# Kernel tuning notes

Measured on AMD Instinct MI355X. Metric: run time of the kernel, lower is better.

## Reference

```python
import jax, jax.numpy as jnp
import numpy as np

B = 8           # hardcoded batchsize in the original forward
EPS = 1e-4      # scn.BatchNormalization default eps


def setup_inputs() -> dict:
    key = jax.random.key(0)
    ks = jax.random.split(key, 8)
    Nq, Nkv = 16384, 32768
    dec_in, enc_in, nf = 64, 64, 128
    nbr = jax.random.randint(ks[2], (Nq, 27), 0, Nq, dtype=jnp.int32)
    # center tap of the 3x3x3 submanifold conv is the point itself
    nbr = nbr.at[:, 13].set(jnp.arange(Nq, dtype=jnp.int32))
    return {
        "x_decoder_feat": jax.random.normal(ks[0], (Nq, dec_in), jnp.float32),
        "x_encoder_feat": jax.random.normal(ks[1], (Nkv, enc_in), jnp.float32),
        "nbr_idx": nbr,
        "W_p1": jax.random.normal(ks[3], (27, dec_in, nf), jnp.float32) * 0.05,
        "W_q": jax.random.normal(ks[4], (nf, nf), jnp.float32) * 0.05,
        "W_k": jax.random.normal(ks[5], (enc_in, nf), jnp.float32) * 0.05,
        "W_v": jax.random.normal(ks[6], (enc_in, nf), jnp.float32) * 0.05,
        "W_trans": jax.random.normal(ks[7], (nf, nf), jnp.float32) * 0.05,
        "gamma": jnp.ones((nf,), jnp.float32),
        "beta": jnp.zeros((nf,), jnp.float32),
    }


def reference(x_decoder_feat, x_encoder_feat, nbr_idx, W_p1, W_q, W_k, W_v,
              W_trans, gamma, beta):
    nf = W_q.shape[1]
    # p1: 3x3x3 submanifold conv = gather 27 neighbors, per-offset matmul, sum
    x_dec = jnp.einsum('nkc,kcf->nf', x_decoder_feat[nbr_idx], W_p1)  # [Nq,nf]
    q = (x_dec @ W_q).reshape(B, -1, nf)            # [B, nq, nf]
    k = (x_encoder_feat @ W_k).reshape(B, -1, nf)   # [B, nkv, nf]
    v = (x_encoder_feat @ W_v).reshape(B, -1, nf)
    # per-batch QK^T softmax V (no 1/sqrt(d) scaling in original)
    attn = jax.nn.softmax(jnp.einsum('bqc,bkc->bqk', q, k), axis=-1)
    x_r = jnp.einsum('bqk,bkc->bqc', attn, v).reshape(-1, nf)  # [Nq,nf]
    # trans_conv (1x1) + batchnorm (batch stats over all points)
    t = x_r @ W_trans
    mean = t.mean(axis=0)
    var = t.var(axis=0)
    bn = (t - mean) * jax.lax.rsqrt(var + EPS) * gamma + beta
    return x_dec + bn
```

## Files before the change

### kernel.cpp

```cpp
#include <hip/hip_runtime.h>
#include <math.h>

#define NQ      16384
#define NKV     32768
#define CIN     64
#define NF      128
#define NOFF    27
#define BATCH   8
#define SQ      2048
#define SKV     4096
#define BN_EPS  1e-4f
#define SPLIT   4
#define KV_PER_SPLIT (SKV / SPLIT)
#define TILES_PER_SPLIT (KV_PER_SPLIT / 64)
#define LOG2E   1.4426950408889634f
#define SHIFT2  57.70780163555854f

typedef unsigned short u16;
typedef unsigned int   u32;
typedef __attribute__((ext_vector_type(4))) float f32x4;
typedef __attribute__((ext_vector_type(8))) short s16x8;

__device__ __forceinline__ u16 f2b(float x) {
    union { float f; unsigned u; } c; c.f = x;
    unsigned r = (c.u + 0x7FFFu + ((c.u >> 16) & 1u)) >> 16;
    return (u16)r;
}
__device__ __forceinline__ float b2f(u16 x) {
    union { unsigned u; float f; } c; c.u = ((unsigned)x) << 16;
    return c.f;
}
__device__ __forceinline__ u32 pk2bf(float lo, float hi) {
    union { float f; u32 u; } a, b;
    a.f = lo; b.f = hi;
    return __builtin_amdgcn_perm(b.u + 0x8000u, a.u + 0x8000u, 0x07060302u);
}
__device__ __forceinline__ void g2l16(const void* gp, void* lp) {
    __builtin_amdgcn_global_load_lds(
        (const __attribute__((address_space(1))) unsigned*)gp,
        (__attribute__((address_space(3))) unsigned*)lp, 16, 0, 0);
}

__device__ __forceinline__ void wtrans_one(
    const float* __restrict__ src, u16* __restrict__ dst, int K, int id, float sc)
{
    int n  = id / (K / 4);
    int k4 = (id % (K / 4)) * 4;
    const float* s = src + (size_t)k4 * NF + n;
    ushort4 o;
    o.x = f2b(s[0] * sc); o.y = f2b(s[NF] * sc);
    o.z = f2b(s[2 * NF] * sc); o.w = f2b(s[3 * NF] * sc);
    *(ushort4*)(dst + (size_t)n * K + k4) = o;
}

__global__ __launch_bounds__(256) void prep_kernel(
    const float* __restrict__ xdec_feat, const float* __restrict__ Wp1,
    const float* __restrict__ Wq, const float* __restrict__ Wk,
    const float* __restrict__ Wv, const float* __restrict__ Wt,
    u16* __restrict__ xf_bf, u16* __restrict__ wp1t,
    u16* __restrict__ wqT, u16* __restrict__ wkT,
    u16* __restrict__ wvT, u16* __restrict__ wtT,
    float* __restrict__ stats)
{
    int bid = blockIdx.x;
    int t   = threadIdx.x;
    if (bid < 1024) {
        int i = (bid * 256 + t) * 4;
        float4 v = *(const float4*)(xdec_feat + i);
        ushort4 o;
        o.x = f2b(v.x); o.y = f2b(v.y); o.z = f2b(v.z); o.w = f2b(v.w);
        *(ushort4*)(xf_bf + i) = o;
    } else if (bid < 1240) {
        int id = (bid - 1024) * 256 + t;
        int ko = id >> 11;
        int r  = id & 2047;
        int f  = r >> 4;
        int c4 = (r & 15) * 4;
        const float* s = Wp1 + (size_t)ko * 8192 + (size_t)c4 * NF + f;
        ushort4 o;
        o.x = f2b(s[0]); o.y = f2b(s[NF]); o.z = f2b(s[2 * NF]); o.w = f2b(s[3 * NF]);
        *(ushort4*)(wp1t + (size_t)ko * 8192 + (size_t)f * 64 + c4) = o;
    } else if (bid < 1288) {
        int id = (bid - 1240) * 256 + t;
        if (id < 4096)        wtrans_one(Wq, wqT, 128, id, LOG2E);
        else if (id < 6144)   wtrans_one(Wk, wkT, 64, id - 4096, 1.f);
        else if (id < 8192)   wtrans_one(Wv, wvT, 64, id - 6144, 1.f);
        else                  wtrans_one(Wt, wtT, 128, id - 8192, 1.f);
    } else {
        stats[t] = 0.f;
    }
}

__global__ __launch_bounds__(256) void main_fused_kernel(
    const float* __restrict__ xenc, const u16* __restrict__ xf,
    const int* __restrict__ nbr, const u16* __restrict__ wp1t,
    const u16* __restrict__ wqT, const u16* __restrict__ wkT,
    const u16* __restrict__ wvT,
    u16* __restrict__ kbuf, u16* __restrict__ vt,
    float* __restrict__ xdec, u16* __restrict__ qbuf)
{
    __shared__ u16 Bs[2][128][64];
    __shared__ int nbr_s[64][28];

    const int t    = threadIdx.x;
    const int w    = t >> 6;
    const int lane = t & 63;
    const int quad = lane >> 4;
    const int l15  = lane & 15;

    if (blockIdx.x < 512) {
        const int m0 = blockIdx.x * 64 + w * 16;
        const float* Ap = xenc + (size_t)(m0 + l15) * CIN + quad * 8;
        float4 a0 = *(const float4*)(Ap);
        float4 a1 = *(const float4*)(Ap + 4);
        float4 a2 = *(const float4*)(Ap + 32);
        float4 a3 = *(const float4*)(Ap + 36);
        union { u16 a[8]; s16x8 v; } p0, p1;
        p0.a[0] = f2b(a0.x); p0.a[1] = f2b(a0.y); p0.a[2] = f2b(a0.z); p0.a[3] = f2b(a0.w);
        p0.a[4] = f2b(a1.x); p0.a[5] = f2b(a1.y); p0.a[6] = f2b(a1.z); p0.a[7] = f2b(a1.w);
        p1.a[0] = f2b(a2.x); p1.a[1] = f2b(a2.y); p1.a[2] = f2b(a2.z); p1.a[3] = f2b(a2.w);
        p1.a[4] = f2b(a3.x); p1.a[5] = f2b(a3.y); p1.a[6] = f2b(a3.z); p1.a[7] = f2b(a3.w);
        s16x8 af0 = p0.v, af1 = p1.v;

        int m  = m0 + quad * 4;
        int bb = m >> 12;
        int kv = m & 4095;
        #pragma unroll
        for (int nt = 0; nt < 8; nt++) {
            f32x4 ka = (f32x4)0.f, va = (f32x4)0.f;
            const u16* Kp = wkT + (size_t)(nt * 16 + l15) * CIN + quad * 8;
            const u16* Vp = wvT + (size_t)(nt * 16 + l15) * CIN + quad * 8;
            s16x8 kb0 = *(const s16x8*)(Kp);
            s16x8 kb1 = *(const s16x8*)(Kp + 32);
            s16x8 vb0 = *(const s16x8*)(Vp);
            s16x8 vb1 = *(const s16x8*)(Vp + 32);
            ka = __builtin_amdgcn_mfma_f32_16x16x32_bf16(af0, kb0, ka, 0, 0, 0);
            ka = __builtin_amdgcn_mfma_f32_16x16x32_bf16(af1, kb1, ka, 0, 0, 0);
            va = __builtin_amdgcn_mfma_f32_16x16x32_bf16(af0, vb0, va, 0, 0, 0);
            va = __builtin_amdgcn_mfma_f32_16x16x32_bf16(af1, vb1, va, 0, 0, 0);
            #pragma unroll
            for (int r = 0; r < 4; r++)
                kbuf[(size_t)(m0 + quad * 4 + r) * NF + nt * 16 + l15] = f2b(ka[r]);
            ushort4 pk;
            pk.x = f2b(va[0]); pk.y = f2b(va[1]); pk.z = f2b(va[2]); pk.w = f2b(va[3]);
            *(ushort4*)(vt + (size_t)(bb * NF + nt * 16 + l15) * SKV + kv) = pk;
        }
        return;
    }

    const int base = (blockIdx.x - 512) * 64;

    for (int i = t; i < 64 * NOFF; i += 256)
        nbr_s[i / NOFF][i % NOFF] = nbr[(size_t)base * NOFF + i];

    f32x4 oacc[8];
    #pragma unroll
    for (int n = 0; n < 8; n++) oacc[n] = (f32x4)0.f;

    const int arow = w * 16 + l15;
    const int sr   = w * 32 + (lane >> 3);

    #pragma unroll
    for (int c = 0; c < 4; c++) {
        int row = sr + c * 8;
        int kk  = (lane & 7) ^ (row & 7);
        g2l16(wp1t + (size_t)row * 64 + kk * 8, &Bs[0][w * 32 + c * 8][0]);
    }
    __syncthreads();

    for (int ko = 0; ko < NOFF; ko++) {
        int cur = ko & 1;
        if (ko + 1 < NOFF) {
            int nxt = (ko + 1) & 1;
            #pragma unroll
            for (int c = 0; c < 4; c++) {
                int row = sr + c * 8;
                int kk  = (lane & 7) ^ (row & 7);
                g2l16(wp1t + (size_t)(ko + 1) * 8192 + (size_t)row * 64 + kk * 8,
                      &Bs[nxt][w * 32 + c * 8][0]);
            }
        }
        int nb = nbr_s[arow][ko];
        const u16* ap = xf + (size_t)nb * CIN + quad * 8;
        s16x8 af0 = *(const s16x8*)(ap);
        s16x8 af1 = *(const s16x8*)(ap + 32);
        #pragma unroll
        for (int nt = 0; nt < 8; nt++) {
            int pc0 = quad ^ (l15 & 7);
            int pc1 = (4 + quad) ^ (l15 & 7);
            s16x8 bf0 = *(const s16x8*)&Bs[cur][nt * 16 + l15][pc0 * 8];
            s16x8 bf1 = *(const s16x8*)&Bs[cur][nt * 16 + l15][pc1 * 8];
            oacc[nt] = __builtin_amdgcn_mfma_f32_16x16x32_bf16(af0, bf0, oacc[nt], 0, 0, 0);
            oacc[nt] = __builtin_amdgcn_mfma_f32_16x16x32_bf16(af1, bf1, oacc[nt], 0, 0, 0);
        }
        __syncthreads();
    }

    u16* xq = &Bs[0][0][0];
    #pragma unroll
    for (int nt = 0; nt < 8; nt++)
        #pragma unroll
        for (int r = 0; r < 4; r++) {
            int row = w * 16 + quad * 4 + r;
            int col = nt * 16 + l15;
            xdec[(size_t)(base + row) * NF + col] = oacc[nt][r];
            xq[row * 136 + col] = f2b(oacc[nt][r]);
        }

    s16x8 aq[4];
    #pragma unroll
    for (int ks = 0; ks < 4; ks++)
        aq[ks] = *(const s16x8*)&xq[(w * 16 + l15) * 136 + ks * 32 + quad * 8];

    #pragma unroll
    for (int nt = 0; nt < 8; nt++) {
        f32x4 acc = (f32x4)0.f;
        const u16* Wp = wqT + (size_t)(nt * 16 + l15) * NF + quad * 8;
        #pragma unroll
        for (int ks = 0; ks < 4; ks++) {
            s16x8 bf = *(const s16x8*)(Wp + ks * 32);
            acc = __builtin_amdgcn_mfma_f32_16x16x32_bf16(aq[ks], bf, acc, 0, 0, 0);
        }
        #pragma unroll
        for (int r = 0; r < 4; r++)
            qbuf[(size_t)(base + w * 16 + quad * 4 + r) * NF + nt * 16 + l15] = f2b(acc[r]);
    }
}

__global__ __launch_bounds__(256) void attn_mfma_kernel(
    const u16* __restrict__ Q, const u16* __restrict__ K,
    const u16* __restrict__ Vt, u16* __restrict__ Opart,
    float* __restrict__ lpart)
{
    __shared__ u16 Ks[2][64][128];
    __shared__ u16 Vs[2][128][64];
    __shared__ u16 Ps[4][16][72];

    const int t    = threadIdx.x;
    const int b    = blockIdx.y;
    const int q0   = blockIdx.x * 128;
    const int sp   = blockIdx.z;
    const int w    = t >> 6;
    const int lane = t & 63;
    const int quad = lane >> 4;
    const int l15  = lane & 15;

    const u16* Kb  = K  + (size_t)b * SKV * NF;
    const u16* Vtb = Vt + (size_t)b * NF * SKV;

    s16x8 qf[2][4];
    #pragma unroll
    for (int g = 0; g < 2; g++) {
        const u16* Qp = Q + ((size_t)(b * SQ + q0 + w * 32 + g * 16 + l15)) * NF + quad * 8;
        #pragma unroll
        for (int ks = 0; ks < 4; ks++) qf[g][ks] = *(const s16x8*)(Qp + ks * 32);
    }

    f32x4 oacc[2][8];
    #pragma unroll
    for (int g = 0; g < 2; g++)
        #pragma unroll
        for (int n = 0; n < 8; n++) oacc[g][n] = (f32x4)0.f;
    float lrow[2] = {0.f, 0.f};

    const int kvbase = sp * KV_PER_SPLIT;
    const int krow = w * 16 + (lane >> 4);
    const int vrow = w * 32 + (lane >> 3);

    #pragma unroll
    for (int c = 0; c < 4; c++) {
        int row = krow + c * 4;
        int k8  = (lane & 15) ^ (row & 15);
        g2l16(Kb + (size_t)(kvbase + row) * NF + k8 * 8, &Ks[0][w * 16 + c * 4][0]);
    }
    #pragma unroll
    for (int c = 0; c < 4; c++) {
        int row = vrow + c * 8;
        int k8  = (lane & 7) ^ (row & 7);
        g2l16(Vtb + (size_t)row * SKV + kvbase + k8 * 8, &Vs[0][w * 32 + c * 8][0]);
    }

    for (int tile = 0; tile < TILES_PER_SPLIT; tile++) {
        const int cur = tile & 1;
        __syncthreads();
        if (tile + 1 < TILES_PER_SPLIT) {
            const int nxt = (tile + 1) & 1;
            int kvn = kvbase + (tile + 1) * 64;
            #pragma unroll
            for (int c = 0; c < 4; c++) {
                int row = krow + c * 4;
                int k8  = (lane & 15) ^ (row & 15);
                g2l16(Kb + (size_t)(kvn + row) * NF + k8 * 8, &Ks[nxt][w * 16 + c * 4][0]);
            }
            #pragma unroll
            for (int c = 0; c < 4; c++) {
                int row = vrow + c * 8;
                int k8  = (lane & 7) ^ (row & 7);
                g2l16(Vtb + (size_t)row * SKV + kvn + k8 * 8, &Vs[nxt][w * 32 + c * 8][0]);
            }
        }

        f32x4 sacc[2][4];
        #pragma unroll
        for (int c = 0; c < 4; c++) {
            sacc[0][c] = (f32x4)0.f;
            sacc[1][c] = (f32x4)0.f;
            #pragma unroll
            for (int ks = 0; ks < 4; ks++) {
                int p = (ks * 4 + quad) ^ l15;
                s16x8 ka = *(const s16x8*)&Ks[cur][c * 16 + l15][p * 8];
                sacc[0][c] = __builtin_amdgcn_mfma_f32_16x16x32_bf16(ka, qf[0][ks], sacc[0][c], 0, 0, 0);
                sacc[1][c] = __builtin_amdgcn_mfma_f32_16x16x32_bf16(ka, qf[1][ks], sacc[1][c], 0, 0, 0);
            }
        }

        s16x8 pb[2][2];
        #pragma unroll
        for (int g = 0; g < 2; g++) {
            float rs = 0.f;
            float pv[4][4];
            #pragma unroll
            for (int c = 0; c < 4; c++)
                #pragma unroll
                for (int r = 0; r < 4; r++) {
                    float p = exp2f(sacc[g][c][r] - SHIFT2);
                    pv[c][r] = p;
                    rs += p;
                }
            rs += __shfl_xor(rs, 16);
            rs += __shfl_xor(rs, 32);
            lrow[g] += rs;
            #pragma unroll
            for (int c = 0; c < 4; c++) {
                uint2 pk;
                pk.x = pk2bf(pv[c][0], pv[c][1]);
                pk.y = pk2bf(pv[c][2], pv[c][3]);
                *(uint2*)&Ps[w][l15][c * 16 + quad * 4] = pk;
            }
            pb[g][0] = *(const s16x8*)&Ps[w][l15][quad * 8];
            pb[g][1] = *(const s16x8*)&Ps[w][l15][32 + quad * 8];
        }

        #pragma unroll
        for (int mt = 0; mt < 8; mt++) {
            int p0 = quad ^ (l15 & 7);
            int p1 = (4 + quad) ^ (l15 & 7);
            s16x8 va0 = *(const s16x8*)&Vs[cur][mt * 16 + l15][p0 * 8];
            s16x8 va1 = *(const s16x8*)&Vs[cur][mt * 16 + l15][p1 * 8];
            oacc[0][mt] = __builtin_amdgcn_mfma_f32_16x16x32_bf16(va0, pb[0][0], oacc[0][mt], 0, 0, 0);
            oacc[0][mt] = __builtin_amdgcn_mfma_f32_16x16x32_bf16(va1, pb[0][1], oacc[0][mt], 0, 0, 0);
            oacc[1][mt] = __builtin_amdgcn_mfma_f32_16x16x32_bf16(va0, pb[1][0], oacc[1][mt], 0, 0, 0);
            oacc[1][mt] = __builtin_amdgcn_mfma_f32_16x16x32_bf16(va1, pb[1][1], oacc[1][mt], 0, 0, 0);
        }
    }

    #pragma unroll
    for (int g = 0; g < 2; g++) {
        int grow = b * SQ + q0 + w * 32 + g * 16 + l15;
        u16* Ob = Opart + (size_t)sp * NQ * NF + (size_t)grow * NF;
        #pragma unroll
        for (int mt = 0; mt < 8; mt++) {
            uint2 ov;
            ov.x = pk2bf(oacc[g][mt][0], oacc[g][mt][1]);
            ov.y = pk2bf(oacc[g][mt][2], oacc[g][mt][3]);
            *(uint2*)(Ob + mt * 16 + quad * 4) = ov;
        }
        if (quad == 0) lpart[sp * NQ + grow] = lrow[g];
    }
}

__global__ __launch_bounds__(256) void tgemm_fused_kernel(
    const u16* __restrict__ Opart, const float* __restrict__ lpart,
    const u16* __restrict__ WT, float* __restrict__ C, float* __restrict__ stats)
{
    const int t    = threadIdx.x;
    const int w    = t >> 6;
    const int lane = t & 63;
    const int quad = lane >> 4;
    const int l15  = lane & 15;
    const int m0   = blockIdx.x * 64 + w * 16;
    const int row  = m0 + l15;

    float L = 0.f;
    #pragma unroll
    for (int s = 0; s < SPLIT; s++) L += lpart[s * NQ + row];
    float invL = 1.f / L;

    s16x8 af[4];
    #pragma unroll
    for (int ks = 0; ks < 4; ks++) {
        float sum[8] = {0.f, 0.f, 0.f, 0.f, 0.f, 0.f, 0.f, 0.f};
        #pragma unroll
        for (int s = 0; s < SPLIT; s++) {
            const u16* p = Opart + (size_t)s * NQ * NF + (size_t)row * NF + ks * 32 + quad * 8;
            ushort4 u0 = *(const ushort4*)p;
            ushort4 u1 = *(const ushort4*)(p + 4);
            sum[0] += b2f(u0.x); sum[1] += b2f(u0.y);
            sum[2] += b2f(u0.z); sum[3] += b2f(u0.w);
            sum[4] += b2f(u1.x); sum[5] += b2f(u1.y);
            sum[6] += b2f(u1.z); sum[7] += b2f(u1.w);
        }
        union { u16 a[8]; s16x8 v; } pk;
        #pragma unroll
        for (int j = 0; j < 8; j++) pk.a[j] = f2b(sum[j] * invL);
        af[ks] = pk.v;
    }

    f32x4 oacc[8];
    #pragma unroll
    for (int nt = 0; nt < 8; nt++) {
        oacc[nt] = (f32x4)0.f;
        const u16* Wp = WT + (size_t)(nt * 16 + l15) * NF + quad * 8;
        #pragma unroll
        for (int ks = 0; ks < 4; ks++) {
            s16x8 bf = *(const s16x8*)(Wp + ks * 32);
            oacc[nt] = __builtin_amdgcn_mfma_f32_16x16x32_bf16(af[ks], bf, oacc[nt], 0, 0, 0);
        }
    }

    float s[8], sq[8];
    #pragma unroll
    for (int nt = 0; nt < 8; nt++) {
        s[nt] = 0.f; sq[nt] = 0.f;
        #pragma unroll
        for (int r = 0; r < 4; r++) {
            float v = oacc[nt][r];
            C[(size_t)(m0 + quad * 4 + r) * NF + nt * 16 + l15] = v;
            s[nt] += v; sq[nt] += v * v;
        }
    }
    #pragma unroll
    for (int nt = 0; nt < 8; nt++) {
        s[nt]  += __shfl_xor(s[nt], 16);  s[nt]  += __shfl_xor(s[nt], 32);
        sq[nt] += __shfl_xor(sq[nt], 16); sq[nt] += __shfl_xor(sq[nt], 32);
    }
    __shared__ float red[2][4][128];
    if (quad == 0) {
        #pragma unroll
        for (int nt = 0; nt < 8; nt++) {
            red[0][w][nt * 16 + l15] = s[nt];
            red[1][w][nt * 16 + l15] = sq[nt];
        }
    }
    __syncthreads();
    if (t < 128) {
        float a = red[0][0][t] + red[0][1][t] + red[0][2][t] + red[0][3][t];
        atomicAdd(&stats[t], a);
    } else if (t < 256) {
        int f = t - 128;
        float a = red[1][0][f] + red[1][1][f] + red[1][2][f] + red[1][3][f];
        atomicAdd(&stats[128 + f], a);
    }
}

__global__ __launch_bounds__(256) void bn_finalize(
    const float* __restrict__ tbuf, const float* __restrict__ xdec,
    const float* __restrict__ stats, const float* __restrict__ gamma,
    const float* __restrict__ beta, float* __restrict__ out)
{
    const int g = blockIdx.x * 256 + threadIdx.x;
    const int e = g * 4;
    const int f = e & (NF - 1);
    const float invN = 1.0f / (float)NQ;
    float4 tv = *(const float4*)(tbuf + e);
    float4 xv = *(const float4*)(xdec + e);
    float o[4], tt[4] = {tv.x, tv.y, tv.z, tv.w}, xx[4] = {xv.x, xv.y, xv.z, xv.w};
    #pragma unroll
    for (int u = 0; u < 4; u++) {
        float sum  = stats[f + u];
        float sumq = stats[128 + f + u];
        float mean = sum * invN;
        float var  = sumq * invN - mean * mean;
        float sc   = rsqrtf(var + BN_EPS) * gamma[f + u];
        o[u] = xx[u] + (tt[u] - mean) * sc + beta[f + u];
    }
    float4 ov = make_float4(o[0], o[1], o[2], o[3]);
    *(float4*)(out + e) = ov;
}

extern "C" void kernel_launch(void* const* d_in, const int* in_sizes, int n_in,
                              void* d_out, int out_size, void* d_ws, size_t ws_size,
                              hipStream_t stream) {
    const float* xdec_feat = (const float*)d_in[0];
    const float* xenc_feat = (const float*)d_in[1];
    const int*   nbr       = (const int*)d_in[2];
    const float* Wp1       = (const float*)d_in[3];
    const float* Wq        = (const float*)d_in[4];
    const float* Wk        = (const float*)d_in[5];
    const float* Wv        = (const float*)d_in[6];
    const float* Wt        = (const float*)d_in[7];
    const float* gamma     = (const float*)d_in[8];
    const float* beta      = (const float*)d_in[9];
    float* out = (float*)d_out;

    char* wsb = (char*)d_ws;
    const size_t MB = 1024 * 1024;
    float* xdec   = (float*)(wsb + 0);
    u16*   qbuf   = (u16*)  (wsb + 8 * MB);
    u16*   kbuf   = (u16*)  (wsb + 12 * MB);
    u16*   vt     = (u16*)  (wsb + 20 * MB);
    u16*   opart  = (u16*)  (wsb + 28 * MB);
    u16*   xf_bf  = (u16*)  (wsb + 44 * MB);
    u16*   wp1t   = (u16*)  (wsb + 46 * MB);
    u16*   wqT    = (u16*)  (wsb + 46 * MB + 512 * 1024);
    u16*   wkT    = (u16*)  (wsb + 46 * MB + 512 * 1024 + 32768);
    u16*   wvT    = (u16*)  (wsb + 46 * MB + 512 * 1024 + 49152);
    u16*   wtT    = (u16*)  (wsb + 46 * MB + 512 * 1024 + 65536);
    float* lpart  = (float*)(wsb + 47 * MB);
    float* stats  = (float*)(wsb + 47 * MB + 512 * 1024);
    float* tbuf   = (float*)(wsb + 12 * MB);

    prep_kernel<<<1289, 256, 0, stream>>>(
        xdec_feat, Wp1, Wq, Wk, Wv, Wt,
        xf_bf, wp1t, wqT, wkT, wvT, wtT, stats);
    main_fused_kernel<<<768, 256, 0, stream>>>(
        xenc_feat, xf_bf, nbr, wp1t, wqT, wkT, wvT,
        kbuf, vt, xdec, qbuf);
    attn_mfma_kernel<<<dim3(SQ / 128, BATCH, SPLIT), 256, 0, stream>>>(
        qbuf, kbuf, vt, opart, lpart);
    tgemm_fused_kernel<<<NQ / 64, 256, 0, stream>>>(opart, lpart, wtT, tbuf, stats);
    bn_finalize<<<(NQ * NF) / 1024, 256, 0, stream>>>(tbuf, xdec, stats, gamma, beta, out);
}
```

Measured before the change: 194.6 us.

## Load K fragments directly from global in attention; stage V^T writes through LDS

The attention kernel stops staging K tiles through double-buffered shared memory. Each wave now reads its K fragments straight from global memory (likely L2-resident, since every wave reads the same tile), which frees LDS and removes those async copies. In the K/V projection blocks, the transposed V output is first assembled in shared memory and then written with coalesced 16-byte stores instead of scattered 8-byte stores. The risk is that global K loads now sit on the critical path of the QK MFMAs without prefetch, and four waves redundantly load the same K rows.

```diff
diff --git a/kernel.cpp b/kernel.cpp
--- a/kernel.cpp
+++ b/kernel.cpp
@@ -99,7 +99,7 @@
     u16* __restrict__ kbuf, u16* __restrict__ vt,
     float* __restrict__ xdec, u16* __restrict__ qbuf)
 {
-    __shared__ u16 Bs[2][128][64];
+    __shared__ u16 smem[2][128][64];
     __shared__ int nbr_s[64][28];
 
     const int t    = threadIdx.x;
@@ -109,7 +109,8 @@
     const int l15  = lane & 15;
 
     if (blockIdx.x < 512) {
-        const int m0 = blockIdx.x * 64 + w * 16;
+        const int bm0 = blockIdx.x * 64;
+        const int m0  = bm0 + w * 16;
         const float* Ap = xenc + (size_t)(m0 + l15) * CIN + quad * 8;
         float4 a0 = *(const float4*)(Ap);
         float4 a1 = *(const float4*)(Ap + 4);
@@ -122,9 +123,7 @@
         p1.a[4] = f2b(a3.x); p1.a[5] = f2b(a3.y); p1.a[6] = f2b(a3.z); p1.a[7] = f2b(a3.w);
         s16x8 af0 = p0.v, af1 = p1.v;
 
-        int m  = m0 + quad * 4;
-        int bb = m >> 12;
-        int kv = m & 4095;
+        u16* vtile = &smem[0][0][0];
         #pragma unroll
         for (int nt = 0; nt < 8; nt++) {
             f32x4 ka = (f32x4)0.f, va = (f32x4)0.f;
@@ -143,7 +142,18 @@
                 kbuf[(size_t)(m0 + quad * 4 + r) * NF + nt * 16 + l15] = f2b(ka[r]);
             ushort4 pk;
             pk.x = f2b(va[0]); pk.y = f2b(va[1]); pk.z = f2b(va[2]); pk.w = f2b(va[3]);
-            *(ushort4*)(vt + (size_t)(bb * NF + nt * 16 + l15) * SKV + kv) = pk;
+            *(ushort4*)&vtile[(nt * 16 + l15) * 64 + w * 16 + quad * 4] = pk;
+        }
+        __syncthreads();
+        int bb  = bm0 >> 12;
+        int kv0 = bm0 & 4095;
+        #pragma unroll
+        for (int it = 0; it < 4; it++) {
+            int idx = it * 256 + t;
+            int row = idx >> 3;
+            int ch  = idx & 7;
+            *(uint4*)(vt + (size_t)(bb * NF + row) * SKV + kv0 + ch * 8) =
+                *(const uint4*)&vtile[row * 64 + ch * 8];
         }
         return;
     }
@@ -164,7 +174,7 @@
     for (int c = 0; c < 4; c++) {
         int row = sr + c * 8;
         int kk  = (lane & 7) ^ (row & 7);
-        g2l16(wp1t + (size_t)row * 64 + kk * 8, &Bs[0][w * 32 + c * 8][0]);
+        g2l16(wp1t + (size_t)row * 64 + kk * 8, &smem[0][w * 32 + c * 8][0]);
     }
     __syncthreads();
 
@@ -177,7 +187,7 @@
                 int row = sr + c * 8;
                 int kk  = (lane & 7) ^ (row & 7);
                 g2l16(wp1t + (size_t)(ko + 1) * 8192 + (size_t)row * 64 + kk * 8,
-                      &Bs[nxt][w * 32 + c * 8][0]);
+                      &smem[nxt][w * 32 + c * 8][0]);
             }
         }
         int nb = nbr_s[arow][ko];
@@ -188,15 +198,15 @@
         for (int nt = 0; nt < 8; nt++) {
             int pc0 = quad ^ (l15 & 7);
             int pc1 = (4 + quad) ^ (l15 & 7);
-            s16x8 bf0 = *(const s16x8*)&Bs[cur][nt * 16 + l15][pc0 * 8];
-            s16x8 bf1 = *(const s16x8*)&Bs[cur][nt * 16 + l15][pc1 * 8];
+            s16x8 bf0 = *(const s16x8*)&smem[cur][nt * 16 + l15][pc0 * 8];
+            s16x8 bf1 = *(const s16x8*)&smem[cur][nt * 16 + l15][pc1 * 8];
             oacc[nt] = __builtin_amdgcn_mfma_f32_16x16x32_bf16(af0, bf0, oacc[nt], 0, 0, 0);
             oacc[nt] = __builtin_amdgcn_mfma_f32_16x16x32_bf16(af1, bf1, oacc[nt], 0, 0, 0);
         }
         __syncthreads();
     }
 
-    u16* xq = &Bs[0][0][0];
+    u16* xq = &smem[0][0][0];
     #pragma unroll
     for (int nt = 0; nt < 8; nt++)
         #pragma unroll
@@ -232,7 +242,6 @@
     const u16* __restrict__ Vt, u16* __restrict__ Opart,
     float* __restrict__ lpart)
 {
-    __shared__ u16 Ks[2][64][128];
     __shared__ u16 Vs[2][128][64];
     __shared__ u16 Ps[4][16][72];
 
@@ -264,15 +273,8 @@
     float lrow[2] = {0.f, 0.f};
 
     const int kvbase = sp * KV_PER_SPLIT;
-    const int krow = w * 16 + (lane >> 4);
     const int vrow = w * 32 + (lane >> 3);
 
-    #pragma unroll
-    for (int c = 0; c < 4; c++) {
-        int row = krow + c * 4;
-        int k8  = (lane & 15) ^ (row & 15);
-        g2l16(Kb + (size_t)(kvbase + row) * NF + k8 * 8, &Ks[0][w * 16 + c * 4][0]);
-    }
     #pragma unroll
     for (int c = 0; c < 4; c++) {
         int row = vrow + c * 8;
@@ -282,16 +284,11 @@
 
     for (int tile = 0; tile < TILES_PER_SPLIT; tile++) {
         const int cur = tile & 1;
+        const int kv0 = kvbase + tile * 64;
         __syncthreads();
         if (tile + 1 < TILES_PER_SPLIT) {
             const int nxt = (tile + 1) & 1;
-            int kvn = kvbase + (tile + 1) * 64;
-            #pragma unroll
-            for (int c = 0; c < 4; c++) {
-                int row = krow + c * 4;
-                int k8  = (lane & 15) ^ (row & 15);
-                g2l16(Kb + (size_t)(kvn + row) * NF + k8 * 8, &Ks[nxt][w * 16 + c * 4][0]);
-            }
+            int kvn = kv0 + 64;
             #pragma unroll
             for (int c = 0; c < 4; c++) {
                 int row = vrow + c * 8;
@@ -303,15 +300,22 @@
         f32x4 sacc[2][4];
         #pragma unroll
         for (int c = 0; c < 4; c++) {
-            sacc[0][c] = (f32x4)0.f;
-            sacc[1][c] = (f32x4)0.f;
-            #pragma unroll
-            for (int ks = 0; ks < 4; ks++) {
-                int p = (ks * 4 + quad) ^ l15;
-                s16x8 ka = *(const s16x8*)&Ks[cur][c * 16 + l15][p * 8];
-                sacc[0][c] = __builtin_amdgcn_mfma_f32_16x16x32_bf16(ka, qf[0][ks], sacc[0][c], 0, 0, 0);
-                sacc[1][c] = __builtin_amdgcn_mfma_f32_16x16x32_bf16(ka, qf[1][ks], sacc[1][c], 0, 0, 0);
-            }
+            const u16* Krow = Kb + (size_t)(kv0 + c * 16 + l15) * NF + quad * 8;
+            s16x8 ka0 = *(const s16x8*)(Krow);
+            s16x8 ka1 = *(const s16x8*)(Krow + 32);
+            s16x8 ka2 = *(const s16x8*)(Krow + 64);
+            s16x8 ka3 = *(const s16x8*)(Krow + 96);
+            f32x4 s0 = (f32x4)0.f, s1 = (f32x4)0.f;
+            s0 = __builtin_amdgcn_mfma_f32_16x16x32_bf16(ka0, qf[0][0], s0, 0, 0, 0);
+            s0 = __builtin_amdgcn_mfma_f32_16x16x32_bf16(ka1, qf[0][1], s0, 0, 0, 0);
+            s0 = __builtin_amdgcn_mfma_f32_16x16x32_bf16(ka2, qf[0][2], s0, 0, 0, 0);
+            s0 = __builtin_amdgcn_mfma_f32_16x16x32_bf16(ka3, qf[0][3], s0, 0, 0, 0);
+            s1 = __builtin_amdgcn_mfma_f32_16x16x32_bf16(ka0, qf[1][0], s1, 0, 0, 0);
+            s1 = __builtin_amdgcn_mfma_f32_16x16x32_bf16(ka1, qf[1][1], s1, 0, 0, 0);
+            s1 = __builtin_amdgcn_mfma_f32_16x16x32_bf16(ka2, qf[1][2], s1, 0, 0, 0);
+            s1 = __builtin_amdgcn_mfma_f32_16x16x32_bf16(ka3, qf[1][3], s1, 0, 0, 0);
+            sacc[0][c] = s0;
+            sacc[1][c] = s1;
         }
 
         s16x8 pb[2][2];
```

Measured after the change: 226.9 us. +16.6%, slower.
